# Optimization experiments

Hardware: AMD Instinct MI355X
Metric: run time of the kernel (lower is better)

Reference implementation:

```python
import jax, jax.numpy as jnp
import numpy as np


def setup_inputs() -> dict:
    key = jax.random.key(0)
    k1, k2 = jax.random.split(key)
    B, EMB, CODES, NUM_TOKENS = 16, 64, 16384, 1024
    x_in = jax.random.normal(k1, (B, EMB, CODES), dtype=jnp.float32)
    code_embedding = jax.random.uniform(k2, (NUM_TOKENS, EMB), dtype=jnp.float32)
    return {"x_in": x_in, "code_embedding": code_embedding}


def reference(x_in, code_embedding):
    # x_in: [B, emb, codes]; code_embedding: [num_tokens, emb]
    x_t = jnp.transpose(x_in, (0, 2, 1))  # [B, codes, emb]
    # squared euclidean distances (argmin is invariant to sqrt used by cdist)
    x2 = jnp.sum(x_t * x_t, axis=-1)                      # [B, codes]
    e2 = jnp.sum(code_embedding * code_embedding, axis=-1)  # [num_tokens]
    dots = jnp.einsum('bce,ke->bck', x_t, code_embedding)   # [B, codes, num_tokens]
    dist2 = x2[:, :, None] - 2.0 * dots + e2[None, None, :]
    indices = jnp.argmin(dist2, axis=2)                   # [B, codes]
    x_out = jnp.transpose(code_embedding[indices], (0, 2, 1))  # [B, emb, codes]
    return x_out, indices[:, :, None]  # indices keepdim like torch argmin(keepdim=True)
```

## Files before the change

kernel.cpp:

```cpp
#include <hip/hip_runtime.h>


#define BB 16
#define EMB 64
#define CODES 16384
#define NT 1024
#define NTILES 64
#define CHUNK 4
#define EPOCHS (NTILES / CHUNK)

typedef __attribute__((ext_vector_type(8))) short s16x8;
typedef __attribute__((ext_vector_type(4))) float f32x4;
typedef __attribute__((ext_vector_type(4))) int i32x4;
typedef unsigned int u32;

__device__ inline short bf16_hi(float f) { return (short)(__builtin_bit_cast(u32, f) >> 16); }
__device__ inline float hi_part(float f) { return __builtin_bit_cast(float, __builtin_bit_cast(u32, f) & 0xFFFF0000u); }
__device__ inline u32 umin_(u32 a, u32 b) { return a < b ? a : b; }
__device__ inline u32 umax_(u32 a, u32 b) { return a > b ? a : b; }

__device__ inline void async_copy16(const char* g, char* lds_base_uniform) {
  __builtin_amdgcn_global_load_lds(
      (const __attribute__((address_space(1))) unsigned int*)g,
      (__attribute__((address_space(3))) unsigned int*)(unsigned int)(unsigned long long)lds_base_uniform,
      16, 0, 0);
}

#define WSE_OFF   0
#define WSH_OFF   266240
#define WSH2_OFF  270336

__global__ __launch_bounds__(256) void vq_prep(const float* __restrict__ E,
                                               char* __restrict__ wsE,
                                               float* __restrict__ wsh,
                                               float* __restrict__ wsh2) {
  const int bid = blockIdx.x, tid = threadIdx.x;
  if (bid < 32) {
    const int gid = bid * 256 + tid;
    const int nt = gid >> 7, ks = (gid >> 6) & 1, lane = gid & 63;
    const int col = lane & 15, quad = lane >> 4;
    const int n = nt * 16 + col;
    const int k0 = ks * 32 + quad * 8;
    const float* ep = E + n * EMB + k0;
    s16x8 hv, lv;
    #pragma unroll
    for (int j = 0; j < 8; ++j) {
      float v = ep[j];
      float hf = hi_part(v);
      hv[j] = bf16_hi(v);
      lv[j] = bf16_hi(v - hf);
    }
    char* base = wsE + ((size_t)nt << 12) + ((size_t)ks << 10) + lane * 16;
    *(i32x4*)(base)        = __builtin_bit_cast(i32x4, hv);
    *(i32x4*)(base + 2048) = __builtin_bit_cast(i32x4, lv);
  } else {
    const int n = (bid - 32) * 256 + tid;
    if (n < NT) {
      const float4* ep = (const float4*)(E + n * EMB);
      float s = 0.f;
      #pragma unroll
      for (int g = 0; g < 16; ++g) { float4 v = ep[g]; s += v.x*v.x + v.y*v.y + v.z*v.z + v.w*v.w; }
      const float h = -0.5f * s;
      wsh[n] = h;
      wsh2[n] = 16384.f * (h + 128.f);
    }
  }
}

__global__ __launch_bounds__(256, 3) void vq_main(
    const float* __restrict__ x, const float* __restrict__ E,
    const char* __restrict__ wsE, const float* __restrict__ wsh,
    const float* __restrict__ wsh2,
    float* __restrict__ xout, float* __restrict__ iout) {
  __shared__ char smem[2 * CHUNK * 4096 + 4096];
  float* lh = (float*)(smem + 2 * CHUNK * 4096);
  const int tid = threadIdx.x;
  const int wave = tid >> 6, lane = tid & 63;
  const int col = lane & 15, quad = lane >> 4;
  const int b = blockIdx.y;
  const int c0 = blockIdx.x * 256;
  const int cw = c0 + wave * 64;

  ((float4*)lh)[tid] = ((const float4*)wsh2)[tid];
  {
    const char* g = wsE + wave * 4096 + lane * 16;
    char* lb = smem + wave * 4096;
    async_copy16(g,        lb);
    async_copy16(g + 1024, lb + 1024);
    async_copy16(g + 2048, lb + 2048);
    async_copy16(g + 3072, lb + 3072);
  }

  s16x8 ah[4][2], al[4][2];
  #pragma unroll
  for (int mt = 0; mt < 4; ++mt) {
    #pragma unroll
    for (int ks = 0; ks < 2; ++ks) {
      s16x8 hv, lv;
      #pragma unroll
      for (int j = 0; j < 8; ++j) {
        const int e = ks * 32 + quad * 8 + j;
        float v = x[((size_t)b * EMB + e) * CODES + (size_t)(cw + mt * 16 + col)] * 16384.f;
        float hf = hi_part(v);
        hv[j] = bf16_hi(v);
        lv[j] = bf16_hi(v - hf);
      }
      ah[mt][ks] = hv;
      al[mt][ks] = lv;
    }
  }

  u32 k1[4][4], k2[4][4];
  #pragma unroll
  for (int mt = 0; mt < 4; ++mt)
    #pragma unroll
    for (int r = 0; r < 4; ++r) { k1[mt][r] = 0u; k2[mt][r] = 0u; }

  u32 inv = 1023u - (u32)col;

  __syncthreads();

  for (int c = 0; c < EPOCHS; ++c) {
    if (c < EPOCHS - 1) {
      const char* g = wsE + (size_t)(c + 1) * (CHUNK * 4096) + wave * 4096 + lane * 16;
      char* lb = smem + ((c + 1) & 1) * (CHUNK * 4096) + wave * 4096;
      async_copy16(g,        lb);
      async_copy16(g + 1024, lb + 1024);
      async_copy16(g + 2048, lb + 2048);
      async_copy16(g + 3072, lb + 3072);
    }

    const char* rb = smem + (c & 1) * (CHUNK * 4096) + lane * 16;
    #pragma unroll
    for (int t = 0; t < CHUNK; ++t) {
      const char* p = rb + t * 4096;
      const s16x8 bh0 = __builtin_bit_cast(s16x8, *(const i32x4*)(p));
      const s16x8 bh1 = __builtin_bit_cast(s16x8, *(const i32x4*)(p + 1024));
      const s16x8 bl0 = __builtin_bit_cast(s16x8, *(const i32x4*)(p + 2048));
      const s16x8 bl1 = __builtin_bit_cast(s16x8, *(const i32x4*)(p + 3072));
      const float ch = lh[(c * CHUNK + t) * 16 + col];
      const f32x4 cq = (f32x4){ch, ch, ch, ch};

      f32x4 acc[4];
      #pragma unroll
      for (int mt = 0; mt < 4; ++mt) {
        acc[mt] = __builtin_amdgcn_mfma_f32_16x16x32_bf16(ah[mt][0], bh0, cq, 0, 0, 0);
        acc[mt] = __builtin_amdgcn_mfma_f32_16x16x32_bf16(ah[mt][1], bh1, acc[mt], 0, 0, 0);
        acc[mt] = __builtin_amdgcn_mfma_f32_16x16x32_bf16(al[mt][0], bh0, acc[mt], 0, 0, 0);
        acc[mt] = __builtin_amdgcn_mfma_f32_16x16x32_bf16(al[mt][1], bh1, acc[mt], 0, 0, 0);
        acc[mt] = __builtin_amdgcn_mfma_f32_16x16x32_bf16(ah[mt][0], bl0, acc[mt], 0, 0, 0);
        acc[mt] = __builtin_amdgcn_mfma_f32_16x16x32_bf16(ah[mt][1], bl1, acc[mt], 0, 0, 0);
      }

      #pragma unroll
      for (int mt = 0; mt < 4; ++mt) {
        #pragma unroll
        for (int r = 0; r < 4; ++r) {
          u32 q = (u32)acc[mt][r];
          u32 key = (q << 10) + inv;
          u32 tt = umin_(key, k1[mt][r]);
          k1[mt][r] = umax_(key, k1[mt][r]);
          k2[mt][r] = umax_(tt, k2[mt][r]);
        }
      }
      inv -= 16u;
    }
    __syncthreads();
  }

  uint2* cand = (uint2*)smem;
  #pragma unroll
  for (int mt = 0; mt < 4; ++mt) {
    #pragma unroll
    for (int r = 0; r < 4; ++r) {
      u32 a1 = k1[mt][r], a2 = k2[mt][r];
      #pragma unroll
      for (int m = 1; m <= 8; m <<= 1) {
        u32 r1 = __shfl_xor(a1, m, 64);
        u32 r2 = __shfl_xor(a2, m, 64);
        u32 t = umin_(a1, r1);
        a1 = umax_(a1, r1);
        a2 = umax_(umax_(a2, r2), t);
      }
      if (col == r) cand[wave * 64 + mt * 16 + quad * 4 + r] = make_uint2(a1, a2);
    }
  }
  __syncthreads();

  const u32 K1 = cand[tid].x, K2 = cand[tid].y;
  const int i1 = 1023 - (int)(K1 & 1023u);
  const int i2 = 1023 - (int)(K2 & 1023u);
  const float* xq = x + (size_t)b * EMB * CODES + (size_t)(c0 + tid);
  const float4* e1 = (const float4*)(E + i1 * EMB);
  const float4* e2 = (const float4*)(E + i2 * EMB);
  float d10 = 0, d11 = 0, d12 = 0, d13 = 0, d20 = 0, d21 = 0, d22 = 0, d23 = 0;
  #pragma unroll
  for (int g = 0; g < 16; ++g) {
    float4 a = e1[g], c4 = e2[g];
    float x0 = xq[(size_t)(4 * g + 0) * CODES];
    float x1 = xq[(size_t)(4 * g + 1) * CODES];
    float x2 = xq[(size_t)(4 * g + 2) * CODES];
    float x3 = xq[(size_t)(4 * g + 3) * CODES];
    d10 = fmaf(x0, a.x, d10);  d11 = fmaf(x1, a.y, d11);
    d12 = fmaf(x2, a.z, d12);  d13 = fmaf(x3, a.w, d13);
    d20 = fmaf(x0, c4.x, d20); d21 = fmaf(x1, c4.y, d21);
    d22 = fmaf(x2, c4.z, d22); d23 = fmaf(x3, c4.w, d23);
  }
  const float s1 = ((d10 + d11) + (d12 + d13)) + wsh[i1];
  const float s2 = ((d20 + d21) + (d22 + d23)) + wsh[i2];
  const bool take2 = (s2 > s1) || (s2 == s1 && i2 < i1);
  const int idx = take2 ? i2 : i1;

  iout[(size_t)b * CODES + (size_t)(c0 + tid)] = (float)idx;
  const float* Er = E + idx * EMB;
  float* xo = xout + (size_t)b * EMB * CODES + (size_t)(c0 + tid);
  #pragma unroll
  for (int e = 0; e < EMB; ++e) xo[(size_t)e * CODES] = Er[e];
}

extern "C" void kernel_launch(void* const* d_in, const int* in_sizes, int n_in,
                              void* d_out, int out_size, void* d_ws, size_t ws_size,
                              hipStream_t stream) {
  const float* x = (const float*)d_in[0];
  const float* E = (const float*)d_in[1];
  float* xout = (float*)d_out;
  float* iout = (float*)d_out + (size_t)BB * EMB * CODES;

  char* wsE  = (char*)d_ws + WSE_OFF;
  float* wsh  = (float*)((char*)d_ws + WSH_OFF);
  float* wsh2 = (float*)((char*)d_ws + WSH2_OFF);

  vq_prep<<<36, 256, 0, stream>>>(E, wsE, wsh, wsh2);
  vq_main<<<dim3(CODES / 256, BB), 256, 0, stream>>>(x, E, wsE, wsh, wsh2, xout, iout);
}
```

Baseline: 203.1 us.

## Switch to single fp16 MFMA pass with top-3 candidate exact rescoring

Replaces the split-bf16 (hi/lo) three-product MFMA scheme with a single fp16 product per k-slice, so each tile needs two MFMAs instead of six and the codebook in the workspace and LDS is half the size. To make up for the lower precision it keeps three best candidates per code instead of two and rescores all three exactly in fp32. Blocks shrink to 128 threads (two waves), each covering 128 codes. The risk is that fp16 with the 4096 scale may lose range or precision so that the true argmin falls outside the top three.

```diff
diff --git a/kernel.cpp b/kernel.cpp
--- a/kernel.cpp
+++ b/kernel.cpp
@@ -8,14 +8,13 @@
 #define NTILES 64
 #define CHUNK 4
 #define EPOCHS (NTILES / CHUNK)
-
-typedef __attribute__((ext_vector_type(8))) short s16x8;
+#define QPB 128
+
+typedef __attribute__((ext_vector_type(8))) _Float16 f16x8;
 typedef __attribute__((ext_vector_type(4))) float f32x4;
 typedef __attribute__((ext_vector_type(4))) int i32x4;
 typedef unsigned int u32;
 
-__device__ inline short bf16_hi(float f) { return (short)(__builtin_bit_cast(u32, f) >> 16); }
-__device__ inline float hi_part(float f) { return __builtin_bit_cast(float, __builtin_bit_cast(u32, f) & 0xFFFF0000u); }
 __device__ inline u32 umin_(u32 a, u32 b) { return a < b ? a : b; }
 __device__ inline u32 umax_(u32 a, u32 b) { return a > b ? a : b; }
 
@@ -27,8 +26,8 @@
 }
 
 #define WSE_OFF   0
-#define WSH_OFF   266240
-#define WSH2_OFF  270336
+#define WSH_OFF   131072
+#define WSH2_OFF  135168
 
 __global__ __launch_bounds__(256) void vq_prep(const float* __restrict__ E,
                                                char* __restrict__ wsE,
@@ -42,17 +41,11 @@
     const int n = nt * 16 + col;
     const int k0 = ks * 32 + quad * 8;
     const float* ep = E + n * EMB + k0;
-    s16x8 hv, lv;
-    #pragma unroll
-    for (int j = 0; j < 8; ++j) {
-      float v = ep[j];
-      float hf = hi_part(v);
-      hv[j] = bf16_hi(v);
-      lv[j] = bf16_hi(v - hf);
-    }
-    char* base = wsE + ((size_t)nt << 12) + ((size_t)ks << 10) + lane * 16;
-    *(i32x4*)(base)        = __builtin_bit_cast(i32x4, hv);
-    *(i32x4*)(base + 2048) = __builtin_bit_cast(i32x4, lv);
+    f16x8 hv;
+    #pragma unroll
+    for (int j = 0; j < 8; ++j) hv[j] = (_Float16)ep[j];
+    char* base = wsE + ((size_t)nt << 11) + ((size_t)ks << 10) + lane * 16;
+    *(i32x4*)(base) = __builtin_bit_cast(i32x4, hv);
   } else {
     const int n = (bid - 32) * 256 + tid;
     if (n < NT) {
@@ -62,59 +55,57 @@
       for (int g = 0; g < 16; ++g) { float4 v = ep[g]; s += v.x*v.x + v.y*v.y + v.z*v.z + v.w*v.w; }
       const float h = -0.5f * s;
       wsh[n] = h;
-      wsh2[n] = 16384.f * (h + 128.f);
-    }
-  }
-}
-
-__global__ __launch_bounds__(256, 3) void vq_main(
+      wsh2[n] = 4096.f * (h + 128.f);
+    }
+  }
+}
+
+__global__ __launch_bounds__(128, 3) void vq_main(
     const float* __restrict__ x, const float* __restrict__ E,
     const char* __restrict__ wsE, const float* __restrict__ wsh,
     const float* __restrict__ wsh2,
     float* __restrict__ xout, float* __restrict__ iout) {
-  __shared__ char smem[2 * CHUNK * 4096 + 4096];
-  float* lh = (float*)(smem + 2 * CHUNK * 4096);
+  __shared__ char smem[2 * CHUNK * 2048 + 4096];
+  float* lh = (float*)(smem + 2 * CHUNK * 2048);
   const int tid = threadIdx.x;
   const int wave = tid >> 6, lane = tid & 63;
   const int col = lane & 15, quad = lane >> 4;
   const int b = blockIdx.y;
-  const int c0 = blockIdx.x * 256;
+  const int c0 = blockIdx.x * QPB;
   const int cw = c0 + wave * 64;
 
   ((float4*)lh)[tid] = ((const float4*)wsh2)[tid];
+  ((float4*)lh)[tid + 128] = ((const float4*)wsh2)[tid + 128];
   {
-    const char* g = wsE + wave * 4096 + lane * 16;
-    char* lb = smem + wave * 4096;
+    const char* g = wsE + (size_t)(wave * 2) * 2048 + lane * 16;
+    char* lb = smem + (wave * 2) * 2048;
     async_copy16(g,        lb);
     async_copy16(g + 1024, lb + 1024);
     async_copy16(g + 2048, lb + 2048);
     async_copy16(g + 3072, lb + 3072);
   }
 
-  s16x8 ah[4][2], al[4][2];
+  f16x8 af[4][2];
   #pragma unroll
   for (int mt = 0; mt < 4; ++mt) {
     #pragma unroll
     for (int ks = 0; ks < 2; ++ks) {
-      s16x8 hv, lv;
+      f16x8 hv;
       #pragma unroll
       for (int j = 0; j < 8; ++j) {
         const int e = ks * 32 + quad * 8 + j;
-        float v = x[((size_t)b * EMB + e) * CODES + (size_t)(cw + mt * 16 + col)] * 16384.f;
-        float hf = hi_part(v);
-        hv[j] = bf16_hi(v);
-        lv[j] = bf16_hi(v - hf);
-      }
-      ah[mt][ks] = hv;
-      al[mt][ks] = lv;
-    }
-  }
-
-  u32 k1[4][4], k2[4][4];
+        float v = x[((size_t)b * EMB + e) * CODES + (size_t)(cw + mt * 16 + col)] * 4096.f;
+        hv[j] = (_Float16)v;
+      }
+      af[mt][ks] = hv;
+    }
+  }
+
+  u32 k1[4][4], k2[4][4], k3[4][4];
   #pragma unroll
   for (int mt = 0; mt < 4; ++mt)
     #pragma unroll
-    for (int r = 0; r < 4; ++r) { k1[mt][r] = 0u; k2[mt][r] = 0u; }
+    for (int r = 0; r < 4; ++r) { k1[mt][r] = 0u; k2[mt][r] = 0u; k3[mt][r] = 0u; }
 
   u32 inv = 1023u - (u32)col;
 
@@ -122,34 +113,28 @@
 
   for (int c = 0; c < EPOCHS; ++c) {
     if (c < EPOCHS - 1) {
-      const char* g = wsE + (size_t)(c + 1) * (CHUNK * 4096) + wave * 4096 + lane * 16;
-      char* lb = smem + ((c + 1) & 1) * (CHUNK * 4096) + wave * 4096;
+      const char* g = wsE + (size_t)((c + 1) * CHUNK + wave * 2) * 2048 + lane * 16;
+      char* lb = smem + ((c + 1) & 1) * (CHUNK * 2048) + (wave * 2) * 2048;
       async_copy16(g,        lb);
       async_copy16(g + 1024, lb + 1024);
       async_copy16(g + 2048, lb + 2048);
       async_copy16(g + 3072, lb + 3072);
     }
 
-    const char* rb = smem + (c & 1) * (CHUNK * 4096) + lane * 16;
+    const char* rb = smem + (c & 1) * (CHUNK * 2048) + lane * 16;
     #pragma unroll
     for (int t = 0; t < CHUNK; ++t) {
-      const char* p = rb + t * 4096;
-      const s16x8 bh0 = __builtin_bit_cast(s16x8, *(const i32x4*)(p));
-      const s16x8 bh1 = __builtin_bit_cast(s16x8, *(const i32x4*)(p + 1024));
-      const s16x8 bl0 = __builtin_bit_cast(s16x8, *(const i32x4*)(p + 2048));
-      const s16x8 bl1 = __builtin_bit_cast(s16x8, *(const i32x4*)(p + 3072));
+      const char* p = rb + t * 2048;
+      const f16x8 b0 = __builtin_bit_cast(f16x8, *(const i32x4*)(p));
+      const f16x8 b1 = __builtin_bit_cast(f16x8, *(const i32x4*)(p + 1024));
       const float ch = lh[(c * CHUNK + t) * 16 + col];
       const f32x4 cq = (f32x4){ch, ch, ch, ch};
 
       f32x4 acc[4];
       #pragma unroll
       for (int mt = 0; mt < 4; ++mt) {
-        acc[mt] = __builtin_amdgcn_mfma_f32_16x16x32_bf16(ah[mt][0], bh0, cq, 0, 0, 0);
-        acc[mt] = __builtin_amdgcn_mfma_f32_16x16x32_bf16(ah[mt][1], bh1, acc[mt], 0, 0, 0);
-        acc[mt] = __builtin_amdgcn_mfma_f32_16x16x32_bf16(al[mt][0], bh0, acc[mt], 0, 0, 0);
-        acc[mt] = __builtin_amdgcn_mfma_f32_16x16x32_bf16(al[mt][1], bh1, acc[mt], 0, 0, 0);
-        acc[mt] = __builtin_amdgcn_mfma_f32_16x16x32_bf16(ah[mt][0], bl0, acc[mt], 0, 0, 0);
-        acc[mt] = __builtin_amdgcn_mfma_f32_16x16x32_bf16(ah[mt][1], bl1, acc[mt], 0, 0, 0);
+        acc[mt] = __builtin_amdgcn_mfma_f32_16x16x32_f16(af[mt][0], b0, cq, 0, 0, 0);
+        acc[mt] = __builtin_amdgcn_mfma_f32_16x16x32_f16(af[mt][1], b1, acc[mt], 0, 0, 0);
       }
 
       #pragma unroll
@@ -158,9 +143,11 @@
         for (int r = 0; r < 4; ++r) {
           u32 q = (u32)acc[mt][r];
           u32 key = (q << 10) + inv;
-          u32 tt = umin_(key, k1[mt][r]);
+          u32 t1 = umin_(key, k1[mt][r]);
           k1[mt][r] = umax_(key, k1[mt][r]);
-          k2[mt][r] = umax_(tt, k2[mt][r]);
+          u32 t2 = umin_(t1, k2[mt][r]);
+          k2[mt][r] = umax_(t1, k2[mt][r]);
+          k3[mt][r] = umax_(t2, k3[mt][r]);
         }
       }
       inv -= 16u;
@@ -168,50 +155,64 @@
     __syncthreads();
   }
 
-  uint2* cand = (uint2*)smem;
+  uint4* cand = (uint4*)smem;
+  int* idxs = (int*)(smem + 2048);
   #pragma unroll
   for (int mt = 0; mt < 4; ++mt) {
     #pragma unroll
     for (int r = 0; r < 4; ++r) {
-      u32 a1 = k1[mt][r], a2 = k2[mt][r];
+      u32 a1 = k1[mt][r], a2 = k2[mt][r], a3 = k3[mt][r];
       #pragma unroll
       for (int m = 1; m <= 8; m <<= 1) {
-        u32 r1 = __shfl_xor(a1, m, 64);
-        u32 r2 = __shfl_xor(a2, m, 64);
-        u32 t = umin_(a1, r1);
-        a1 = umax_(a1, r1);
-        a2 = umax_(umax_(a2, r2), t);
-      }
-      if (col == r) cand[wave * 64 + mt * 16 + quad * 4 + r] = make_uint2(a1, a2);
+        u32 b1 = __shfl_xor(a1, m, 64);
+        u32 b2 = __shfl_xor(a2, m, 64);
+        u32 b3 = __shfl_xor(a3, m, 64);
+        u32 y1 = umin_(a1, b1);
+        u32 x2 = umax_(a2, b2);
+        u32 m3 = umax_(a3, b3);
+        a1 = umax_(a1, b1);
+        a2 = umax_(y1, x2);
+        a3 = umax_(umin_(y1, x2), umin_(umax_(y1, x2), m3));
+      }
+      if (col == r) cand[wave * 64 + mt * 16 + quad * 4 + r] = make_uint4(a1, a2, a3, 0);
     }
   }
   __syncthreads();
 
-  const u32 K1 = cand[tid].x, K2 = cand[tid].y;
-  const int i1 = 1023 - (int)(K1 & 1023u);
-  const int i2 = 1023 - (int)(K2 & 1023u);
+  const uint4 K = cand[tid];
+  const int i1 = 1023 - (int)(K.x & 1023u);
+  const int i2 = 1023 - (int)(K.y & 1023u);
+  const int i3 = 1023 - (int)(K.z & 1023u);
   const float* xq = x + (size_t)b * EMB * CODES + (size_t)(c0 + tid);
   const float4* e1 = (const float4*)(E + i1 * EMB);
   const float4* e2 = (const float4*)(E + i2 * EMB);
-  float d10 = 0, d11 = 0, d12 = 0, d13 = 0, d20 = 0, d21 = 0, d22 = 0, d23 = 0;
+  const float4* e3 = (const float4*)(E + i3 * EMB);
+  float d1 = 0.f, d2 = 0.f, d3 = 0.f;
+  float d1b = 0.f, d2b = 0.f, d3b = 0.f;
   #pragma unroll
   for (int g = 0; g < 16; ++g) {
-    float4 a = e1[g], c4 = e2[g];
+    float4 a = e1[g], c4 = e2[g], f4 = e3[g];
     float x0 = xq[(size_t)(4 * g + 0) * CODES];
     float x1 = xq[(size_t)(4 * g + 1) * CODES];
     float x2 = xq[(size_t)(4 * g + 2) * CODES];
     float x3 = xq[(size_t)(4 * g + 3) * CODES];
-    d10 = fmaf(x0, a.x, d10);  d11 = fmaf(x1, a.y, d11);
-    d12 = fmaf(x2, a.z, d12);  d13 = fmaf(x3, a.w, d13);
-    d20 = fmaf(x0, c4.x, d20); d21 = fmaf(x1, c4.y, d21);
-    d22 = fmaf(x2, c4.z, d22); d23 = fmaf(x3, c4.w, d23);
-  }
-  const float s1 = ((d10 + d11) + (d12 + d13)) + wsh[i1];
-  const float s2 = ((d20 + d21) + (d22 + d23)) + wsh[i2];
-  const bool take2 = (s2 > s1) || (s2 == s1 && i2 < i1);
-  const int idx = take2 ? i2 : i1;
-
+    d1  = fmaf(x0, a.x, d1);   d1b = fmaf(x1, a.y, d1b);
+    d1  = fmaf(x2, a.z, d1);   d1b = fmaf(x3, a.w, d1b);
+    d2  = fmaf(x0, c4.x, d2);  d2b = fmaf(x1, c4.y, d2b);
+    d2  = fmaf(x2, c4.z, d2);  d2b = fmaf(x3, c4.w, d2b);
+    d3  = fmaf(x0, f4.x, d3);  d3b = fmaf(x1, f4.y, d3b);
+    d3  = fmaf(x2, f4.z, d3);  d3b = fmaf(x3, f4.w, d3b);
+  }
+  const float s1 = (d1 + d1b) + wsh[i1];
+  const float s2 = (d2 + d2b) + wsh[i2];
+  const float s3 = (d3 + d3b) + wsh[i3];
+  float bs = s1; int bi = i1;
+  if (s2 > bs || (s2 == bs && i2 < bi)) { bs = s2; bi = i2; }
+  if (s3 > bs || (s3 == bs && i3 < bi)) { bs = s3; bi = i3; }
+  const int idx = bi;
+  idxs[tid] = idx;
   iout[(size_t)b * CODES + (size_t)(c0 + tid)] = (float)idx;
+
   const float* Er = E + idx * EMB;
   float* xo = xout + (size_t)b * EMB * CODES + (size_t)(c0 + tid);
   #pragma unroll
@@ -231,5 +232,5 @@
   float* wsh2 = (float*)((char*)d_ws + WSH2_OFF);
 
   vq_prep<<<36, 256, 0, stream>>>(E, wsE, wsh, wsh2);
-  vq_main<<<dim3(CODES / 256, BB), 256, 0, stream>>>(x, E, wsE, wsh, wsh2, xout, iout);
-}
+  vq_main<<<dim3(CODES / QPB, BB), 128, 0, stream>>>(x, E, wsE, wsh, wsh2, xout, iout);
+}
```

After: 223.6 us. +10.1%, slower.
